# Kernel tuning notes

Hardware: AMD Instinct MI355X
Metric: run time of the kernel (lower is better)

The kernel has to match this reference:

```python
import jax, jax.numpy as jnp
import numpy as np

PAD = 0.1
RESO = 128           # plane_resolution
HID = 128            # hidden_dim
CDIM = 128           # c_dim
NBLK = 5             # n_blocks
PLANES = (('xz', (0, 2)), ('xy', (0, 1)), ('yz', (1, 2)))


def normalize_coordinate(p, dims):
    # p: (B,T,3) -> (B,T,2) in [0, 1)
    xy = p[..., list(dims)] / (1.0 + PAD + 1e-3) + 0.5
    return jnp.clip(xy, 0.0, 1.0 - 1e-5)


def coordinate2index(xy, reso):
    g = (xy * reso).astype(jnp.int32)          # (B,T,2)
    return g[..., 0] + reso * g[..., 1]        # (B,T) flat cell index


def scatter_max_gather(vals, idx, n_cells):
    # vals: (B,T,F), idx: (B,T) -> per-cell max gathered back to points (B,T,F)
    B, T, F = vals.shape
    flat_idx = (idx + jnp.arange(B, dtype=idx.dtype)[:, None] * n_cells).reshape(-1)
    fea = jax.ops.segment_max(vals.reshape(B * T, F), flat_idx, num_segments=B * n_cells)
    return fea[flat_idx].reshape(B, T, F)


def scatter_mean_plane(c, idx, n_cells):
    # c: (B,T,C), idx: (B,T) -> (B, n_cells, C); empty cells stay 0
    B, T, C = c.shape
    flat_idx = (idx + jnp.arange(B, dtype=idx.dtype)[:, None] * n_cells).reshape(-1)
    s = jax.ops.segment_sum(c.reshape(B * T, C), flat_idx, num_segments=B * n_cells)
    cnt = jax.ops.segment_sum(jnp.ones((B * T,), c.dtype), flat_idx, num_segments=B * n_cells)
    return (s / jnp.maximum(cnt, 1.0)[:, None]).reshape(B, n_cells, C)


def resnet_block(x, W0, b0, W1, b1, Ws):
    # ResnetBlockFC(2H -> H), size_h = H, shortcut = Linear(no bias)
    net = jax.nn.relu(x) @ W0 + b0
    dx = jax.nn.relu(net) @ W1 + b1
    return x @ Ws + dx


def setup_inputs() -> dict:
    key = jax.random.key(0)
    ks = jax.random.split(key, 10)
    B, T = 2, 32768
    s = 0.05
    return {
        'p': jax.random.uniform(ks[0], (B, T, 3), jnp.float32, -0.5, 0.5),
        'fc_pos_W': s * jax.random.normal(ks[1], (3, 2 * HID), jnp.float32),
        'fc_pos_b': s * jax.random.normal(ks[2], (2 * HID,), jnp.float32),
        'blocks_W0': s * jax.random.normal(ks[3], (NBLK, 2 * HID, HID), jnp.float32),
        'blocks_b0': s * jax.random.normal(ks[4], (NBLK, HID), jnp.float32),
        'blocks_W1': s * jax.random.normal(ks[5], (NBLK, HID, HID), jnp.float32),
        'blocks_b1': s * jax.random.normal(ks[6], (NBLK, HID), jnp.float32),
        'blocks_Ws': s * jax.random.normal(ks[7], (NBLK, 2 * HID, HID), jnp.float32),
        'fc_c_W': s * jax.random.normal(ks[8], (HID, CDIM), jnp.float32),
        'fc_c_b': s * jax.random.normal(ks[9], (CDIM,), jnp.float32),
    }


def reference(p, fc_pos_W, fc_pos_b, blocks_W0, blocks_b0, blocks_W1, blocks_b1,
              blocks_Ws, fc_c_W, fc_c_b):
    B, T, _ = p.shape
    R2 = RESO * RESO
    index = {k: coordinate2index(normalize_coordinate(p, d), RESO) for k, d in PLANES}

    net = p @ fc_pos_W + fc_pos_b                       # (B,T,2H)
    net = resnet_block(net, blocks_W0[0], blocks_b0[0],
                       blocks_W1[0], blocks_b1[0], blocks_Ws[0])  # (B,T,H)
    for i in range(1, NBLK):
        pooled = sum(scatter_max_gather(net, index[k], R2) for k, _ in PLANES)
        net = jnp.concatenate([net, pooled], axis=-1)   # (B,T,2H)
        net = resnet_block(net, blocks_W0[i], blocks_b0[i],
                           blocks_W1[i], blocks_b1[i], blocks_Ws[i])

    c = net @ fc_c_W + fc_c_b                           # (B,T,C)
    planes = []
    for k, _ in PLANES:  # order: xz, xy, yz
        fea = scatter_mean_plane(c, index[k], R2)       # (B,R2,C)
        planes.append(fea.transpose(0, 2, 1).reshape(B, CDIM, RESO, RESO))
    return jnp.stack(planes)                            # (3,B,C,R,R)
```

## Files before the change

### kernel.cpp

```cpp
#include <hip/hip_runtime.h>

#define TT 65536
#define R2 16384

typedef _Float16 f16x8 __attribute__((ext_vector_type(8)));
typedef float    f32x4 __attribute__((ext_vector_type(4)));
typedef unsigned u32x4 __attribute__((ext_vector_type(4)));

#define MFMA16 __builtin_amdgcn_mfma_f32_16x16x32_f16

#define LTS 136
#define LTW 2176

__device__ __forceinline__ unsigned short f2h(float f){
    _Float16 h = (_Float16)f;
    return __builtin_bit_cast(unsigned short, h);
}
__device__ __forceinline__ float h2f(unsigned short u){
    return (float)__builtin_bit_cast(_Float16, u);
}
__device__ __forceinline__ unsigned relu2(unsigned w){
    unsigned s = w & 0x80008000u;
    unsigned mask = ((s >> 15) * 0x7FFFu) | s;
    return w & ~mask;
}
__device__ __forceinline__ float nrm(float a){
    float v = a / 1.101f + 0.5f;
    v = fmaxf(v, 0.0f);
    v = fminf(v, 0.99999f);
    return v;
}
#define VMCNT0() asm volatile("s_waitcnt vmcnt(0)" ::: "memory")
#define LGKM0()  asm volatile("s_waitcnt lgkmcnt(0)" ::: "memory")

__global__ __launch_bounds__(256) void k_repack(const float* __restrict__ W0,
        const float* __restrict__ W1, const float* __restrict__ Ws,
        const float* __restrict__ Wc, unsigned short* __restrict__ out,
        int* __restrict__ cnt){
    __shared__ unsigned short lh[4096];
    int b = blockIdx.x, tid = threadIdx.x;

    int gid = b*256 + tid;
    if (gid < 24576){ u32x4 z = {0,0,0,0}; ((u32x4*)cnt)[gid] = z; }

    const float* src; int obase;
    if (b < 100){
        int i = b/20, rr = b%20;
        if (rr < 8){       src = W0 + (size_t)i*32768 + rr*4096;      obase = i*81920 + rr*4096; }
        else if (rr < 12){ int ks=rr-8;  src = W1 + (size_t)i*16384 + ks*4096; obase = i*81920 + 32768 + ks*4096; }
        else {             int ks=rr-12; src = Ws + (size_t)i*32768 + ks*4096; obase = i*81920 + 49152 + ks*4096; }
    } else { int ks = b-100; src = Wc + ks*4096; obase = 409600 + ks*4096; }

    #pragma unroll
    for (int m = 0; m < 16; m++){
        int gi = m*256 + tid;
        lh[gi] = f2h(src[gi]);
    }
    __syncthreads();

    #pragma unroll
    for (int g2 = 0; g2 < 2; g2++){
        int base = tid*16 + g2*8;
        int l = (base >> 3) & 63, t = (base >> 9) & 7;
        int n = t*16 + (l & 15), kb = (l >> 4)*8;
        unsigned short h[8];
        #pragma unroll
        for (int j = 0; j < 8; j++) h[j] = lh[(kb + j)*128 + n];
        u32x4 pk;
        #pragma unroll
        for (int q = 0; q < 4; q++)
            pk[q] = (unsigned)h[2*q] | ((unsigned)h[2*q+1] << 16);
        *(u32x4*)(&out[obase + base]) = pk;
    }
}

__global__ __launch_bounds__(256) void k_idxhist(const float* __restrict__ p,
        int* __restrict__ idx, int* __restrict__ cnt){
    int pt = blockIdx.x*256 + threadIdx.x;
    float p0 = p[pt*3+0], p1 = p[pt*3+1], p2 = p[pt*3+2];
    int g0 = (int)(nrm(p0)*128.f);
    int g1 = (int)(nrm(p1)*128.f);
    int g2 = (int)(nrm(p2)*128.f);
    int i0 = g0 + 128*g2, i1 = g0 + 128*g1, i2 = g1 + 128*g2;
    idx[0*TT + pt] = i0;
    idx[1*TT + pt] = i1;
    idx[2*TT + pt] = i2;
    int b14 = (pt >> 15) << 14;
    atomicAdd(&cnt[0*32768 + b14 + i0], 1);
    atomicAdd(&cnt[1*32768 + b14 + i1], 1);
    atomicAdd(&cnt[2*32768 + b14 + i2], 1);
}

__global__ __launch_bounds__(1024) void k_scan(const int* cnt,
        int* __restrict__ cs, int* cp){
    __shared__ int wsum[16];
    int pl = blockIdx.x, tid = threadIdx.x;
    int lane = tid & 63, wid = tid >> 6;
    const int* c = cnt + pl*32768;
    int v[32], tot = 0;
    #pragma unroll
    for (int j = 0; j < 32; j++){ v[j] = c[tid*32 + j]; tot += v[j]; }
    int x = tot;
    #pragma unroll
    for (int off = 1; off < 64; off <<= 1){
        int y = __shfl_up(x, off, 64);
        if (lane >= off) x += y;
    }
    if (lane == 63) wsum[wid] = x;
    __syncthreads();
    int woff = 0;
    #pragma unroll
    for (int j = 0; j < 16; j++) woff += (j < wid) ? wsum[j] : 0;
    int run = woff + x - tot;
    #pragma unroll
    for (int j = 0; j < 32; j++){
        cs[pl*32769 + tid*32 + j] = run;
        cp[pl*32768 + tid*32 + j] = run;
        run += v[j];
    }
    if (tid == 1023) cs[pl*32769 + 32768] = TT;
}

__global__ __launch_bounds__(256) void k_scatter(const int* __restrict__ idx,
        int* __restrict__ cp, int* __restrict__ srt){
    int pt = blockIdx.x*256 + threadIdx.x;
    int b14 = (pt >> 15) << 14;
    #pragma unroll
    for (int pl = 0; pl < 3; pl++){
        int pos = atomicAdd(&cp[pl*32768 + b14 + idx[pl*TT + pt]], 1);
        srt[pl*TT + pos] = pt;
    }
}

__global__ __launch_bounds__(256) void k_pool3(const unsigned short* __restrict__ xb,
        const int* __restrict__ srt, const int* __restrict__ cs,
        unsigned short* __restrict__ mxp){
    int pl = blockIdx.y;
    const int* srtp = srt + (size_t)pl*TT;
    const int* csp  = cs  + (size_t)pl*32769;
    int lane = threadIdx.x & 63, w = threadIdx.x >> 6;
    int g = lane >> 4, l16 = lane & 15;
    int cbase = (blockIdx.x*4 + w)*4;
    for (int c = cbase; c < cbase + 4; c++){
        int s = csp[c], e = csp[c+1];
        if (s == e) continue;
        f16x8 m;
        #pragma unroll
        for (int j = 0; j < 8; j++) m[j] = (_Float16)(-65504.f);
        for (int i = s + g; i < e; i += 4){
            int pt = srtp[i];
            f16x8 v = *(const f16x8*)(xb + (size_t)pt*128 + l16*8);
            #pragma unroll
            for (int j = 0; j < 8; j++)
                m[j] = (v[j] > m[j]) ? v[j] : m[j];
        }
        #pragma unroll
        for (int sh = 16; sh <= 32; sh += 16){
            u32x4 um = __builtin_bit_cast(u32x4, m);
            u32x4 o;
            #pragma unroll
            for (int q = 0; q < 4; q++) o[q] = __shfl_xor(um[q], sh, 64);
            f16x8 vm = __builtin_bit_cast(f16x8, o);
            #pragma unroll
            for (int j = 0; j < 8; j++)
                m[j] = (vm[j] > m[j]) ? vm[j] : m[j];
        }
        if (g == 0)
            ((u32x4*)(mxp + ((size_t)pl*32768 + c)*128))[l16] =
                __builtin_bit_cast(u32x4, m);
    }
}

template<int MODE>
__device__ __forceinline__ void resnet_body(
        const unsigned short* __restrict__ xin,
        unsigned short* __restrict__ xout,
        const unsigned short* __restrict__ wp,
        const float* __restrict__ b0, const float* __restrict__ b1,
        const int* __restrict__ idx, const unsigned short* __restrict__ mxp,
        const float* __restrict__ pin, const float* __restrict__ fW,
        const float* __restrict__ fb,
        const unsigned short* __restrict__ wc, const float* __restrict__ bc,
        unsigned short* lw, unsigned short* lt){
    int tid = threadIdx.x, w = tid >> 6, lane = tid & 63;
    int quad = lane >> 4, l15 = lane & 15;
    int m0 = blockIdx.x*64 + w*16;
    unsigned short* ltw = lt + w*LTW;

    auto stage = [&](const unsigned short* src){
        #pragma unroll
        for (int i = 0; i < 8; i++){
            int chunk = i*4 + w;
            __builtin_amdgcn_global_load_lds(
                (const __attribute__((address_space(1))) unsigned*)(src + chunk*512 + lane*8),
                (__attribute__((address_space(3))) unsigned*)(lw + chunk*512),
                16, 0, 0);
        }
    };
    auto gemm = [&](const f16x8* a, f32x4 (&ac)[8]){
        #pragma unroll
        for (int ks = 0; ks < 4; ks++){
            #pragma unroll
            for (int t = 0; t < 8; t++){
                f16x8 b = *(const f16x8*)&lw[((ks*8 + t)*64 + lane)*8];
                ac[t] = MFMA16(a[ks], b, ac[t], 0, 0, 0);
            }
        }
    };

    stage(wp);

    u32x4 xf[4]; f16x8 pf[4];
    if (MODE == 0){
        int row = m0 + l15;
        float p0 = pin[row*3+0], p1 = pin[row*3+1], p2 = pin[row*3+2];
        #pragma unroll
        for (int ks = 0; ks < 4; ks++){
            int c0 = ks*32 + quad*8;
            unsigned short hx[8], hp[8];
            #pragma unroll
            for (int h = 0; h < 2; h++){
                f32x4 w0 = *(const f32x4*)(fW + c0 + h*4);
                f32x4 w1 = *(const f32x4*)(fW + 256 + c0 + h*4);
                f32x4 w2 = *(const f32x4*)(fW + 512 + c0 + h*4);
                f32x4 bb = *(const f32x4*)(fb + c0 + h*4);
                f32x4 v0 = *(const f32x4*)(fW + 128 + c0 + h*4);
                f32x4 v1 = *(const f32x4*)(fW + 384 + c0 + h*4);
                f32x4 v2 = *(const f32x4*)(fW + 640 + c0 + h*4);
                f32x4 bp = *(const f32x4*)(fb + 128 + c0 + h*4);
                #pragma unroll
                for (int j = 0; j < 4; j++){
                    hx[h*4+j] = f2h(bb[j] + p0*w0[j] + p1*w1[j] + p2*w2[j]);
                    hp[h*4+j] = f2h(bp[j] + p0*v0[j] + p1*v1[j] + p2*v2[j]);
                }
            }
            unsigned short* dx = (unsigned short*)&xf[ks];
            unsigned short* dp = (unsigned short*)&pf[ks];
            #pragma unroll
            for (int j = 0; j < 8; j++){ dx[j] = hx[j]; dp[j] = hp[j]; }
        }
    } else {
        int row = m0 + l15;
        size_t rb = (size_t)row*128;
        #pragma unroll
        for (int ks = 0; ks < 4; ks++)
            xf[ks] = *(const u32x4*)(xin + rb + ks*32 + quad*8);
        int b14 = (row >> 15) << 14;
        const unsigned short* q0 = mxp + ((size_t)(0*32768 + b14 + idx[row]))*128;
        const unsigned short* q1 = mxp + ((size_t)(1*32768 + b14 + idx[TT + row]))*128;
        const unsigned short* q2 = mxp + ((size_t)(2*32768 + b14 + idx[2*TT + row]))*128;
        #pragma unroll
        for (int ks = 0; ks < 4; ks++){
            int col = ks*32 + quad*8;
            f16x8 a = *(const f16x8*)(q0 + col);
            f16x8 b = *(const f16x8*)(q1 + col);
            f16x8 c = *(const f16x8*)(q2 + col);
            pf[ks] = a + b + c;
        }
    }

    f32x4 acc[8];
    #pragma unroll
    for (int t = 0; t < 8; t++){ f32x4 z = {0.f,0.f,0.f,0.f}; acc[t] = z; }

    VMCNT0(); __syncthreads();

    {
        f16x8 a[4];
        #pragma unroll
        for (int ks = 0; ks < 4; ks++){
            u32x4 u = xf[ks];
            u.x = relu2(u.x); u.y = relu2(u.y); u.z = relu2(u.z); u.w = relu2(u.w);
            a[ks] = __builtin_bit_cast(f16x8, u);
        }
        gemm(a, acc);
    }
    __syncthreads();
    stage(wp + 16384);
    VMCNT0(); __syncthreads();

    {
        f16x8 a[4];
        #pragma unroll
        for (int ks = 0; ks < 4; ks++){
            u32x4 u = __builtin_bit_cast(u32x4, pf[ks]);
            u.x = relu2(u.x); u.y = relu2(u.y); u.z = relu2(u.z); u.w = relu2(u.w);
            a[ks] = __builtin_bit_cast(f16x8, u);
        }
        gemm(a, acc);
    }
    __syncthreads();
    stage(wp + 32768);
    VMCNT0(); __syncthreads();

    {
        float b0v[8];
        #pragma unroll
        for (int t = 0; t < 8; t++) b0v[t] = b0[t*16 + l15];
        #pragma unroll
        for (int t = 0; t < 8; t++)
            #pragma unroll
            for (int r = 0; r < 4; r++){
                float v = fmaxf(acc[t][r] + b0v[t], 0.f);
                ltw[(quad*4 + r)*LTS + t*16 + l15] = f2h(v);
            }
    }
    LGKM0();
    f32x4 acc2[8];
    {
        #pragma unroll
        for (int t = 0; t < 8; t++){
            float bv = b1[t*16 + l15];
            f32x4 iv = {bv, bv, bv, bv};
            acc2[t] = iv;
        }
    }
    #pragma unroll
    for (int ks = 0; ks < 4; ks++){
        f16x8 a0 = *(const f16x8*)&ltw[l15*LTS + ks*32 + quad*8];
        #pragma unroll
        for (int t = 0; t < 8; t++){
            f16x8 b = *(const f16x8*)&lw[((ks*8 + t)*64 + lane)*8];
            acc2[t] = MFMA16(a0, b, acc2[t], 0, 0, 0);
        }
    }
    __syncthreads();
    stage(wp + 49152);
    VMCNT0(); __syncthreads();

    {
        f16x8 a[4];
        #pragma unroll
        for (int ks = 0; ks < 4; ks++)
            a[ks] = __builtin_bit_cast(f16x8, xf[ks]);
        gemm(a, acc2);
    }
    __syncthreads();
    stage(wp + 65536);
    VMCNT0(); __syncthreads();

    gemm(pf, acc2);

    if (MODE != 2){
        #pragma unroll
        for (int t = 0; t < 8; t++)
            #pragma unroll
            for (int r = 0; r < 4; r++){
                int row = m0 + quad*4 + r;
                xout[(size_t)row*128 + t*16 + l15] = f2h(acc2[t][r]);
            }
        return;
    }
    __syncthreads();
    stage(wc);
    VMCNT0(); __syncthreads();

    #pragma unroll
    for (int t = 0; t < 8; t++)
        #pragma unroll
        for (int r = 0; r < 4; r++)
            ltw[(quad*4 + r)*LTS + t*16 + l15] = f2h(acc2[t][r]);
    LGKM0();
    f32x4 acc3[8];
    #pragma unroll
    for (int t = 0; t < 8; t++){
        float bv = bc[t*16 + l15];
        f32x4 iv = {bv, bv, bv, bv};
        acc3[t] = iv;
    }
    #pragma unroll
    for (int ks = 0; ks < 4; ks++){
        f16x8 a0 = *(const f16x8*)&ltw[l15*LTS + ks*32 + quad*8];
        #pragma unroll
        for (int t = 0; t < 8; t++){
            f16x8 b = *(const f16x8*)&lw[((ks*8 + t)*64 + lane)*8];
            acc3[t] = MFMA16(a0, b, acc3[t], 0, 0, 0);
        }
    }
    #pragma unroll
    for (int t = 0; t < 8; t++)
        #pragma unroll
        for (int r = 0; r < 4; r++){
            int row = m0 + quad*4 + r;
            xout[(size_t)row*128 + t*16 + l15] = f2h(acc3[t][r]);
        }
}

__global__ __launch_bounds__(256, 2) void k_resnet_head(
        unsigned short* __restrict__ xout, const unsigned short* __restrict__ wp,
        const float* __restrict__ b0, const float* __restrict__ b1,
        const float* __restrict__ pin, const float* __restrict__ fW,
        const float* __restrict__ fb){
    __shared__ __align__(16) unsigned short lw[16384];
    __shared__ __align__(16) unsigned short lt[8704];
    resnet_body<0>(nullptr, xout, wp, b0, b1, nullptr, nullptr,
                   pin, fW, fb, nullptr, nullptr, lw, lt);
}
__global__ __launch_bounds__(256, 3) void k_resnet_mid(
        const unsigned short* __restrict__ xin, unsigned short* __restrict__ xout,
        const unsigned short* __restrict__ wp,
        const float* __restrict__ b0, const float* __restrict__ b1,
        const int* __restrict__ idx, const unsigned short* __restrict__ mxp){
    __shared__ __align__(16) unsigned short lw[16384];
    __shared__ __align__(16) unsigned short lt[8704];
    resnet_body<1>(xin, xout, wp, b0, b1, idx, mxp,
                   nullptr, nullptr, nullptr, nullptr, nullptr, lw, lt);
}
__global__ __launch_bounds__(256, 3) void k_resnet_tail(
        const unsigned short* __restrict__ xin, unsigned short* __restrict__ xout,
        const unsigned short* __restrict__ wp,
        const float* __restrict__ b0, const float* __restrict__ b1,
        const int* __restrict__ idx, const unsigned short* __restrict__ mxp,
        const unsigned short* __restrict__ wc, const float* __restrict__ bc){
    __shared__ __align__(16) unsigned short lw[16384];
    __shared__ __align__(16) unsigned short lt[8704];
    resnet_body<2>(xin, xout, wp, b0, b1, idx, mxp,
                   nullptr, nullptr, nullptr, wc, bc, lw, lt);
}

__global__ __launch_bounds__(256) void k_psum3(const unsigned short* __restrict__ cb,
        const int* __restrict__ srt, const int* __restrict__ cs,
        float* __restrict__ out){
    __shared__ float ls[32*129];
    int pl = blockIdx.y;
    const int* srtp = srt + (size_t)pl*TT;
    const int* csp  = cs  + (size_t)pl*32769;
    int tid = threadIdx.x;
    int lane = tid & 63, w = tid >> 6;
    int g = lane >> 4, l16 = lane & 15;
    int c0 = blockIdx.x * 32;
    for (int cc = w*8; cc < w*8 + 8; cc++){
        int c = c0 + cc;
        int s = csp[c], e = csp[c+1];
        float fs[8];
        #pragma unroll
        for (int j = 0; j < 8; j++) fs[j] = 0.f;
        for (int i = s + g; i < e; i += 4){
            int pt = srtp[i];
            u32x4 v = *(const u32x4*)(cb + (size_t)pt*128 + l16*8);
            #pragma unroll
            for (int q = 0; q < 4; q++){
                unsigned u = v[q];
                fs[2*q]   += h2f((unsigned short)(u & 0xFFFF));
                fs[2*q+1] += h2f((unsigned short)(u >> 16));
            }
        }
        #pragma unroll
        for (int j = 0; j < 8; j++){
            fs[j] += __shfl_xor(fs[j], 16, 64);
            fs[j] += __shfl_xor(fs[j], 32, 64);
        }
        float rc = (e > s) ? 1.f/(float)(e - s) : 0.f;
        if (g == 0){
            #pragma unroll
            for (int j = 0; j < 8; j++) ls[cc*129 + l16*8 + j] = fs[j]*rc;
        }
    }
    __syncthreads();
    int pb = pl*2 + (c0 >> 14);
    float* o = out + (size_t)pb*128*R2 + (c0 & 16383);
    #pragma unroll
    for (int k = 0; k < 16; k++){
        int lin = k*256 + tid;
        int f = lin >> 5, cc = lin & 31;
        o[(size_t)f*R2 + cc] = ls[cc*129 + f];
    }
}

extern "C" void kernel_launch(void* const* d_in, const int* in_sizes, int n_in,
                              void* d_out, int out_size, void* d_ws, size_t ws_size,
                              hipStream_t stream) {
    const float* p        = (const float*)d_in[0];
    const float* fc_pos_W = (const float*)d_in[1];
    const float* fc_pos_b = (const float*)d_in[2];
    const float* bW0      = (const float*)d_in[3];
    const float* bb0      = (const float*)d_in[4];
    const float* bW1      = (const float*)d_in[5];
    const float* bb1      = (const float*)d_in[6];
    const float* bWs      = (const float*)d_in[7];
    const float* fc_c_W   = (const float*)d_in[8];
    const float* fc_c_b   = (const float*)d_in[9];
    float* out = (float*)d_out;

    char* ws = (char*)d_ws;
    int*            idx   = (int*)ws;
    unsigned short* net0  = (unsigned short*)(ws + 786432);
    unsigned short* net1  = (unsigned short*)(ws + 17563648);
    unsigned short* cbuf  = (unsigned short*)(ws + 34340864);
    int*            srt   = (int*)(ws + 51118080);
    int*            cs    = (int*)(ws + 51904512);
    int*            cp    = (int*)(ws + 52297744);
    unsigned short* wpack = (unsigned short*)(ws + 52690960);
    unsigned short* mxp   = (unsigned short*)(ws + 53542928);

    k_repack <<<104, 256, 0, stream>>>(bW0, bW1, bWs, fc_c_W, wpack, cp);
    k_idxhist<<<256, 256, 0, stream>>>(p, idx, cp);
    k_scan   <<<3, 1024, 0, stream>>>(cp, cs, cp);
    k_scatter<<<256, 256, 0, stream>>>(idx, cp, srt);

    k_resnet_head<<<1024, 256, 0, stream>>>(net0, wpack, bb0, bb1,
            p, fc_pos_W, fc_pos_b);

    k_pool3<<<dim3(2048, 3), 256, 0, stream>>>(net0, srt, cs, mxp);
    k_resnet_mid<<<1024, 256, 0, stream>>>(net0, net1, wpack + 81920,
            bb0 + 128, bb1 + 128, idx, mxp);
    k_pool3<<<dim3(2048, 3), 256, 0, stream>>>(net1, srt, cs, mxp);
    k_resnet_mid<<<1024, 256, 0, stream>>>(net1, net0, wpack + 163840,
            bb0 + 256, bb1 + 256, idx, mxp);
    k_pool3<<<dim3(2048, 3), 256, 0, stream>>>(net0, srt, cs, mxp);
    k_resnet_mid<<<1024, 256, 0, stream>>>(net0, net1, wpack + 245760,
            bb0 + 384, bb1 + 384, idx, mxp);
    k_pool3<<<dim3(2048, 3), 256, 0, stream>>>(net1, srt, cs, mxp);
    k_resnet_tail<<<1024, 256, 0, stream>>>(net1, cbuf, wpack + 327680,
            bb0 + 512, bb1 + 512, idx, mxp, wpack + 409600, fc_c_b);

    k_psum3<<<dim3(1024, 3), 256, 0, stream>>>(cbuf, srt, cs, out);
}
```

Measured before the change: 382.8 us.

## Use 8-wave blocks for mid/tail resnet and overlap pooled gathers with first GEMM

```diff
diff --git a/kernel.cpp b/kernel.cpp
--- a/kernel.cpp
+++ b/kernel.cpp
@@ -32,6 +32,7 @@
 }
 #define VMCNT0() asm volatile("s_waitcnt vmcnt(0)" ::: "memory")
 #define LGKM0()  asm volatile("s_waitcnt lgkmcnt(0)" ::: "memory")
+#define SB0()    __builtin_amdgcn_sched_barrier(0)
 
 __global__ __launch_bounds__(256) void k_repack(const float* __restrict__ W0,
         const float* __restrict__ W1, const float* __restrict__ Ws,
@@ -171,7 +172,7 @@
     }
 }
 
-template<int MODE>
+template<int MODE, int NW>
 __device__ __forceinline__ void resnet_body(
         const unsigned short* __restrict__ xin,
         unsigned short* __restrict__ xout,
@@ -184,13 +185,13 @@
         unsigned short* lw, unsigned short* lt){
     int tid = threadIdx.x, w = tid >> 6, lane = tid & 63;
     int quad = lane >> 4, l15 = lane & 15;
-    int m0 = blockIdx.x*64 + w*16;
+    int m0 = blockIdx.x*(NW*16) + w*16;
     unsigned short* ltw = lt + w*LTW;
 
     auto stage = [&](const unsigned short* src){
         #pragma unroll
-        for (int i = 0; i < 8; i++){
-            int chunk = i*4 + w;
+        for (int i = 0; i < 32/NW; i++){
+            int chunk = i*NW + w;
             __builtin_amdgcn_global_load_lds(
                 (const __attribute__((address_space(1))) unsigned*)(src + chunk*512 + lane*8),
                 (__attribute__((address_space(3))) unsigned*)(lw + chunk*512),
@@ -209,8 +210,10 @@
     };
 
     stage(wp);
+    SB0();
 
     u32x4 xf[4]; f16x8 pf[4];
+    u32x4 g0[4], g1[4], g2[4];
     if (MODE == 0){
         int row = m0 + l15;
         float p0 = pin[row*3+0], p1 = pin[row*3+1], p2 = pin[row*3+2];
@@ -252,10 +255,9 @@
         #pragma unroll
         for (int ks = 0; ks < 4; ks++){
             int col = ks*32 + quad*8;
-            f16x8 a = *(const f16x8*)(q0 + col);
-            f16x8 b = *(const f16x8*)(q1 + col);
-            f16x8 c = *(const f16x8*)(q2 + col);
-            pf[ks] = a + b + c;
+            g0[ks] = *(const u32x4*)(q0 + col);
+            g1[ks] = *(const u32x4*)(q1 + col);
+            g2[ks] = *(const u32x4*)(q2 + col);
         }
     }
 
@@ -263,7 +265,14 @@
     #pragma unroll
     for (int t = 0; t < 8; t++){ f32x4 z = {0.f,0.f,0.f,0.f}; acc[t] = z; }
 
-    VMCNT0(); __syncthreads();
+    if (MODE == 0){
+        VMCNT0();
+    } else {
+        SB0();
+        asm volatile("s_waitcnt vmcnt(16)" ::: "memory");
+        SB0();
+    }
+    __syncthreads();
 
     {
         f16x8 a[4];
@@ -274,6 +283,15 @@
             a[ks] = __builtin_bit_cast(f16x8, u);
         }
         gemm(a, acc);
+    }
+    if (MODE != 0){
+        #pragma unroll
+        for (int ks = 0; ks < 4; ks++){
+            f16x8 a = __builtin_bit_cast(f16x8, g0[ks]);
+            f16x8 b = __builtin_bit_cast(f16x8, g1[ks]);
+            f16x8 c = __builtin_bit_cast(f16x8, g2[ks]);
+            pf[ks] = a + b + c;
+        }
     }
     __syncthreads();
     stage(wp + 16384);
@@ -393,28 +411,28 @@
         const float* __restrict__ fb){
     __shared__ __align__(16) unsigned short lw[16384];
     __shared__ __align__(16) unsigned short lt[8704];
-    resnet_body<0>(nullptr, xout, wp, b0, b1, nullptr, nullptr,
+    resnet_body<0,4>(nullptr, xout, wp, b0, b1, nullptr, nullptr,
                    pin, fW, fb, nullptr, nullptr, lw, lt);
 }
-__global__ __launch_bounds__(256, 3) void k_resnet_mid(
+__global__ __launch_bounds__(512, 2) void k_resnet_mid(
         const unsigned short* __restrict__ xin, unsigned short* __restrict__ xout,
         const unsigned short* __restrict__ wp,
         const float* __restrict__ b0, const float* __restrict__ b1,
         const int* __restrict__ idx, const unsigned short* __restrict__ mxp){
     __shared__ __align__(16) unsigned short lw[16384];
-    __shared__ __align__(16) unsigned short lt[8704];
-    resnet_body<1>(xin, xout, wp, b0, b1, idx, mxp,
+    __shared__ __align__(16) unsigned short lt[17408];
+    resnet_body<1,8>(xin, xout, wp, b0, b1, idx, mxp,
                    nullptr, nullptr, nullptr, nullptr, nullptr, lw, lt);
 }
-__global__ __launch_bounds__(256, 3) void k_resnet_tail(
+__global__ __launch_bounds__(512, 2) void k_resnet_tail(
         const unsigned short* __restrict__ xin, unsigned short* __restrict__ xout,
         const unsigned short* __restrict__ wp,
         const float* __restrict__ b0, const float* __restrict__ b1,
         const int* __restrict__ idx, const unsigned short* __restrict__ mxp,
         const unsigned short* __restrict__ wc, const float* __restrict__ bc){
     __shared__ __align__(16) unsigned short lw[16384];
-    __shared__ __align__(16) unsigned short lt[8704];
-    resnet_body<2>(xin, xout, wp, b0, b1, idx, mxp,
+    __shared__ __align__(16) unsigned short lt[17408];
+    resnet_body<2,8>(xin, xout, wp, b0, b1, idx, mxp,
                    nullptr, nullptr, nullptr, wc, bc, lw, lt);
 }
 
@@ -502,16 +520,16 @@
             p, fc_pos_W, fc_pos_b);
 
     k_pool3<<<dim3(2048, 3), 256, 0, stream>>>(net0, srt, cs, mxp);
-    k_resnet_mid<<<1024, 256, 0, stream>>>(net0, net1, wpack + 81920,
+    k_resnet_mid<<<512, 512, 0, stream>>>(net0, net1, wpack + 81920,
             bb0 + 128, bb1 + 128, idx, mxp);
     k_pool3<<<dim3(2048, 3), 256, 0, stream>>>(net1, srt, cs, mxp);
-    k_resnet_mid<<<1024, 256, 0, stream>>>(net1, net0, wpack + 163840,
+    k_resnet_mid<<<512, 512, 0, stream>>>(net1, net0, wpack + 163840,
             bb0 + 256, bb1 + 256, idx, mxp);
     k_pool3<<<dim3(2048, 3), 256, 0, stream>>>(net0, srt, cs, mxp);
-    k_resnet_mid<<<1024, 256, 0, stream>>>(net0, net1, wpack + 245760,
+    k_resnet_mid<<<512, 512, 0, stream>>>(net0, net1, wpack + 245760,
             bb0 + 384, bb1 + 384, idx, mxp);
     k_pool3<<<dim3(2048, 3), 256, 0, stream>>>(net1, srt, cs, mxp);
-    k_resnet_tail<<<1024, 256, 0, stream>>>(net1, cbuf, wpack + 327680,
+    k_resnet_tail<<<512, 512, 0, stream>>>(net1, cbuf, wpack + 327680,
             bb0 + 512, bb1 + 512, idx, mxp, wpack + 409600, fc_c_b);
 
     k_psum3<<<dim3(1024, 3), 256, 0, stream>>>(cbuf, srt, cs, out);
```

After: 362.1 us, median of 2. 1.06x faster.
